# Kernel optimization log

Measured on AMD Instinct MI355X. Metric: run time of the kernel, lower is better.

## Reference

```python
import jax, jax.numpy as jnp
import numpy as np

N_NODES = 100000
N_EDGES = 600000
F_IN = 128
F_OUT = 128


def setup_inputs() -> dict:
    key = jax.random.key(0)
    ks = jax.random.split(key, 9)
    stdv = 1.0 / np.sqrt(F_OUT)
    return {
        "x": jax.random.normal(ks[0], (N_NODES, F_IN), dtype=jnp.float32),
        "weight": jax.random.uniform(ks[1], (F_IN, F_OUT), dtype=jnp.float32, minval=-stdv, maxval=stdv),
        "bias": jax.random.uniform(ks[2], (F_OUT,), dtype=jnp.float32, minval=-stdv, maxval=stdv),
        "vals0": jax.random.uniform(ks[3], (N_EDGES,), dtype=jnp.float32),
        "vals1": jax.random.uniform(ks[4], (N_EDGES,), dtype=jnp.float32),
        "rows0": jax.random.randint(ks[5], (N_EDGES,), 0, N_NODES, dtype=jnp.int32),
        "cols0": jax.random.randint(ks[6], (N_EDGES,), 0, N_NODES, dtype=jnp.int32),
        "rows1": jax.random.randint(ks[7], (N_EDGES,), 0, N_NODES, dtype=jnp.int32),
        "cols1": jax.random.randint(ks[8], (N_EDGES,), 0, N_NODES, dtype=jnp.int32),
    }


def _spmm(rows, cols, vals, dense, n):
    # COO sparse [n,n] @ dense [n,f]: gather source rows, scale, scatter-add to dest rows
    msgs = dense[cols] * vals[:, None]          # [E, f]
    return jax.ops.segment_sum(msgs, rows, num_segments=n)


def reference(x, weight, bias, vals0, vals1, rows0, cols0, rows1, cols1):
    n = x.shape[0]
    support = x @ weight                         # [N, F_OUT] dense GEMM
    out = _spmm(rows0, cols0, vals0, support, n) \
        + _spmm(rows1, cols1, vals1, support, n)
    return out + bias
```

## Files before the change

kernel.cpp:

```cpp
#include <hip/hip_runtime.h>


#define FDIM 128
#define EPB 2048

typedef __attribute__((ext_vector_type(8))) short short8;
typedef __attribute__((ext_vector_type(4))) float floatx4;

__device__ __forceinline__ unsigned short f32_to_bf16(float f) {
    unsigned int u = __float_as_uint(f);
    unsigned int r = u + 0x7fffu + ((u >> 16) & 1u);
    return (unsigned short)(r >> 16);
}

__device__ __forceinline__ float bf16_lo(unsigned int u) {
    return __uint_as_float((u & 0xffffu) << 16);
}
__device__ __forceinline__ float bf16_hi(unsigned int u) {
    return __uint_as_float(u & 0xffff0000u);
}

__global__ __launch_bounds__(256) void hist_prep(const int* __restrict__ rows0,
                                                 const int* __restrict__ rows1,
                                                 int* __restrict__ count,
                                                 int* __restrict__ rank, int E,
                                                 const float* __restrict__ w,
                                                 unsigned short* __restrict__ wt,
                                                 int HB) {
    int bid = blockIdx.x;
    if (bid < HB) {
        int gid = bid * 256 + threadIdx.x;
        if (gid < 2 * E) {
            int r = (gid < E) ? rows0[gid] : rows1[gid - E];
            rank[gid] = atomicAdd(&count[r], 1);
        }
    } else {
        int idx = (bid - HB) * 256 + threadIdx.x;
        int nn = idx >> 7, k = idx & 127;
        wt[idx] = f32_to_bf16(w[(size_t)k * FDIM + nn]);
    }
}

__device__ __forceinline__ int block_incl_scan(int v, int tid, int* lds) {
    int lane = tid & 63, wv = tid >> 6;
    #pragma unroll
    for (int d = 1; d < 64; d <<= 1) {
        int y = __shfl_up(v, d);
        if (lane >= d) v += y;
    }
    if (lane == 63) lds[wv] = v;
    __syncthreads();
    if (wv == 0 && lane < 4) {
        int s = lds[lane];
        #pragma unroll
        for (int d = 1; d < 4; d <<= 1) {
            int y = __shfl_up(s, d);
            if (lane >= d) s += y;
        }
        lds[4 + lane] = s;
    }
    __syncthreads();
    int add = (wv > 0) ? lds[4 + wv - 1] : 0;
    return v + add;
}

__global__ __launch_bounds__(256) void rowptr_scan(const int* __restrict__ count,
                                                   int* __restrict__ rowptr,
                                                   int* __restrict__ gcur, int n) {
    __shared__ int lds[8];
    __shared__ int base;
    int tid = threadIdx.x;
    int idx = blockIdx.x * 256 + tid;
    int v = (idx < n) ? count[idx] : 0;
    int inc = block_incl_scan(v, tid, lds);
    if (tid == 255) base = atomicAdd(gcur, inc);
    __syncthreads();
    if (idx < n) rowptr[idx] = base + inc - v;
}

__global__ __launch_bounds__(256) void gemm_lds(const float* __restrict__ x,
                                                const unsigned short* __restrict__ wt,
                                                unsigned short* __restrict__ support,
                                                int n) {
    __shared__ __align__(16) short Bs[128][136];
    const int tid = threadIdx.x;

    #pragma unroll
    for (int i = 0; i < 8; ++i) {
        int idx = tid + i * 256;
        int r = idx >> 4, c8 = idx & 15;
        *(short8*)&Bs[r][c8 * 8] = *(const short8*)(wt + (size_t)r * FDIM + c8 * 8);
    }
    __syncthreads();

    const int wv = tid >> 6, lane = tid & 63;
    const int quad = lane >> 4, lr = lane & 15;
    const int row0 = blockIdx.x * 64 + wv * 16;
    if (row0 >= n) return;

    const int arow = row0 + lr;
    const bool rowok = arow < n;
    const float* xr = x + (size_t)arow * FDIM;

    float4 f[8];
    #pragma unroll
    for (int ks = 0; ks < 4; ++ks) {
        f[2 * ks]     = rowok ? *(const float4*)(xr + ks * 32 + quad * 8)     : make_float4(0.f,0.f,0.f,0.f);
        f[2 * ks + 1] = rowok ? *(const float4*)(xr + ks * 32 + quad * 8 + 4) : make_float4(0.f,0.f,0.f,0.f);
    }

    floatx4 acc[8];
    #pragma unroll
    for (int nt = 0; nt < 8; ++nt) acc[nt] = (floatx4)0.f;

    #pragma unroll
    for (int ks = 0; ks < 4; ++ks) {
        float4 lo = f[2 * ks], hi = f[2 * ks + 1];
        short8 a;
        a[0] = (short)f32_to_bf16(lo.x); a[1] = (short)f32_to_bf16(lo.y);
        a[2] = (short)f32_to_bf16(lo.z); a[3] = (short)f32_to_bf16(lo.w);
        a[4] = (short)f32_to_bf16(hi.x); a[5] = (short)f32_to_bf16(hi.y);
        a[6] = (short)f32_to_bf16(hi.z); a[7] = (short)f32_to_bf16(hi.w);
        #pragma unroll
        for (int nt = 0; nt < 8; ++nt) {
            short8 b = *(const short8*)&Bs[nt * 16 + lr][ks * 32 + quad * 8];
            acc[nt] = __builtin_amdgcn_mfma_f32_16x16x32_bf16(a, b, acc[nt], 0, 0, 0);
        }
    }

    #pragma unroll
    for (int i = 0; i < 4; ++i) {
        int row = row0 + quad * 4 + i;
        if (row < n) {
            #pragma unroll
            for (int nt = 0; nt < 8; ++nt)
                support[(size_t)row * FDIM + nt * 16 + lr] = f32_to_bf16(acc[nt][i]);
        }
    }
}

__global__ __launch_bounds__(256) void scatter_row(
    const int* __restrict__ rows0, const int* __restrict__ cols0, const float* __restrict__ vals0,
    const int* __restrict__ rows1, const int* __restrict__ cols1, const float* __restrict__ vals1,
    const int* __restrict__ rank, const int* __restrict__ rowptr,
    int2* __restrict__ rec, int E, int nper) {
    const int p = blockIdx.x & 7;
    const int rlo = p * nper;
    const int base = (blockIdx.x >> 3) * EPB;
    const int tid = threadIdx.x;
    #pragma unroll
    for (int it = 0; it < EPB / 256; ++it) {
        int gid = base + it * 256 + tid;
        if (gid < 2 * E) {
            int r = (gid < E) ? rows0[gid] : rows1[gid - E];
            if ((unsigned)(r - rlo) < (unsigned)nper) {
                int c; float v;
                if (gid < E) { c = cols0[gid]; v = vals0[gid]; }
                else         { int e = gid - E; c = cols1[e]; v = vals1[e]; }
                rec[rowptr[r] + rank[gid]] = make_int2(c, __float_as_int(v));
            }
        }
    }
}

__global__ __launch_bounds__(256) void pull_csr(const unsigned short* __restrict__ support,
                                                const int* __restrict__ rowptr,
                                                const int* __restrict__ count,
                                                const int2* __restrict__ rec,
                                                const float* __restrict__ bias,
                                                float* __restrict__ out, int n) {
    int wid = (blockIdx.x * 256 + threadIdx.x) >> 6;
    int lane = threadIdx.x & 63;
    if (wid >= n) return;
    int beg = rowptr[wid];
    int end = beg + count[wid];
    float ax = 0.f, ay = 0.f;
    const char* sp = (const char*)support;
    const unsigned loff = (unsigned)lane << 2;

    for (int base = beg; base < end; base += 64) {
        int m = end - base; if (m > 64) m = 64;
        long long pk = 0;
        if (lane < m) pk = *(const long long*)&rec[base + lane];
        int j = 0;
        for (; j + 8 <= m; j += 8) {
            long long p0 = __shfl(pk, j);
            long long p1 = __shfl(pk, j + 1);
            long long p2 = __shfl(pk, j + 2);
            long long p3 = __shfl(pk, j + 3);
            long long p4 = __shfl(pk, j + 4);
            long long p5 = __shfl(pk, j + 5);
            long long p6 = __shfl(pk, j + 6);
            long long p7 = __shfl(pk, j + 7);
            unsigned u0 = *(const unsigned*)(sp + (((unsigned)p0) << 8) + loff);
            unsigned u1 = *(const unsigned*)(sp + (((unsigned)p1) << 8) + loff);
            unsigned u2 = *(const unsigned*)(sp + (((unsigned)p2) << 8) + loff);
            unsigned u3 = *(const unsigned*)(sp + (((unsigned)p3) << 8) + loff);
            unsigned u4 = *(const unsigned*)(sp + (((unsigned)p4) << 8) + loff);
            unsigned u5 = *(const unsigned*)(sp + (((unsigned)p5) << 8) + loff);
            unsigned u6 = *(const unsigned*)(sp + (((unsigned)p6) << 8) + loff);
            unsigned u7 = *(const unsigned*)(sp + (((unsigned)p7) << 8) + loff);
            float v0 = __int_as_float((int)(p0 >> 32));
            float v1 = __int_as_float((int)(p1 >> 32));
            float v2 = __int_as_float((int)(p2 >> 32));
            float v3 = __int_as_float((int)(p3 >> 32));
            float v4 = __int_as_float((int)(p4 >> 32));
            float v5 = __int_as_float((int)(p5 >> 32));
            float v6 = __int_as_float((int)(p6 >> 32));
            float v7 = __int_as_float((int)(p7 >> 32));
            ax += v0 * bf16_lo(u0); ay += v0 * bf16_hi(u0);
            ax += v1 * bf16_lo(u1); ay += v1 * bf16_hi(u1);
            ax += v2 * bf16_lo(u2); ay += v2 * bf16_hi(u2);
            ax += v3 * bf16_lo(u3); ay += v3 * bf16_hi(u3);
            ax += v4 * bf16_lo(u4); ay += v4 * bf16_hi(u4);
            ax += v5 * bf16_lo(u5); ay += v5 * bf16_hi(u5);
            ax += v6 * bf16_lo(u6); ay += v6 * bf16_hi(u6);
            ax += v7 * bf16_lo(u7); ay += v7 * bf16_hi(u7);
        }
        for (; j + 4 <= m; j += 4) {
            long long p0 = __shfl(pk, j);
            long long p1 = __shfl(pk, j + 1);
            long long p2 = __shfl(pk, j + 2);
            long long p3 = __shfl(pk, j + 3);
            unsigned u0 = *(const unsigned*)(sp + (((unsigned)p0) << 8) + loff);
            unsigned u1 = *(const unsigned*)(sp + (((unsigned)p1) << 8) + loff);
            unsigned u2 = *(const unsigned*)(sp + (((unsigned)p2) << 8) + loff);
            unsigned u3 = *(const unsigned*)(sp + (((unsigned)p3) << 8) + loff);
            float v0 = __int_as_float((int)(p0 >> 32));
            float v1 = __int_as_float((int)(p1 >> 32));
            float v2 = __int_as_float((int)(p2 >> 32));
            float v3 = __int_as_float((int)(p3 >> 32));
            ax += v0 * bf16_lo(u0); ay += v0 * bf16_hi(u0);
            ax += v1 * bf16_lo(u1); ay += v1 * bf16_hi(u1);
            ax += v2 * bf16_lo(u2); ay += v2 * bf16_hi(u2);
            ax += v3 * bf16_lo(u3); ay += v3 * bf16_hi(u3);
        }
        for (; j < m; ++j) {
            long long p = __shfl(pk, j);
            unsigned u = *(const unsigned*)(sp + (((unsigned)p) << 8) + loff);
            float v = __int_as_float((int)(p >> 32));
            ax += v * bf16_lo(u); ay += v * bf16_hi(u);
        }
    }
    float2 b = *(const float2*)(bias + lane * 2);
    *(float2*)(out + (size_t)wid * FDIM + lane * 2) = make_float2(ax + b.x, ay + b.y);
}

__global__ __launch_bounds__(256) void wt_only(const float* __restrict__ w,
                                               unsigned short* __restrict__ wt) {
    int idx = blockIdx.x * 256 + threadIdx.x;
    int nn = idx >> 7, k = idx & 127;
    wt[idx] = f32_to_bf16(w[(size_t)k * FDIM + nn]);
}

__global__ __launch_bounds__(256) void init_bias(const float* __restrict__ bias,
                                                 float* __restrict__ out, int n) {
    int idx = blockIdx.x * 256 + threadIdx.x;
    int total = n * (FDIM / 4);
    if (idx < total) {
        int j = (idx & (FDIM / 4 - 1)) * 4;
        float4 b = *(const float4*)(bias + j);
        *(float4*)(out + (size_t)idx * 4) = b;
    }
}

__global__ __launch_bounds__(256) void scatter_bf16(
    const unsigned short* __restrict__ support,
    const int* __restrict__ rows0, const int* __restrict__ cols0, const float* __restrict__ vals0,
    const int* __restrict__ rows1, const int* __restrict__ cols1, const float* __restrict__ vals1,
    float* __restrict__ out, int E) {
    int gid = blockIdx.x * 256 + threadIdx.x;
    int lane = gid & 63;
    int eg = gid >> 6;
    if (eg >= 2 * E) return;
    int r, c; float v;
    if (eg < E) { r = rows0[eg]; c = cols0[eg]; v = vals0[eg]; }
    else        { int e = eg - E; r = rows1[e]; c = cols1[e]; v = vals1[e]; }
    unsigned int u = *(const unsigned int*)(support + (size_t)c * FDIM + lane * 2);
    float sx = bf16_lo(u);
    float sy = bf16_hi(u);
    float* op = out + (size_t)r * FDIM + lane * 2;
    atomicAdd(op,     sx * v);
    atomicAdd(op + 1, sy * v);
}

static inline size_t align256(size_t v) { return (v + 255) & ~(size_t)255; }

extern "C" void kernel_launch(void* const* d_in, const int* in_sizes, int n_in,
                              void* d_out, int out_size, void* d_ws, size_t ws_size,
                              hipStream_t stream) {
    const float* x     = (const float*)d_in[0];
    const float* w     = (const float*)d_in[1];
    const float* bias  = (const float*)d_in[2];
    const float* vals0 = (const float*)d_in[3];
    const float* vals1 = (const float*)d_in[4];
    const int*   rows0 = (const int*)d_in[5];
    const int*   cols0 = (const int*)d_in[6];
    const int*   rows1 = (const int*)d_in[7];
    const int*   cols1 = (const int*)d_in[8];
    const int n = in_sizes[0] / FDIM;
    const int E = in_sizes[3];
    float* out = (float*)d_out;

    const int NB = (n + 255) / 256;

    size_t off = 0;
    unsigned short* support = (unsigned short*)((char*)d_ws + off);
    off = align256(off + (size_t)n * FDIM * 2);
    unsigned short* wt = (unsigned short*)((char*)d_ws + off);
    off = align256(off + (size_t)FDIM * FDIM * 2);
    size_t count_off = off;
    int*  count  = (int*)((char*)d_ws + off);  off = align256(off + (size_t)n * 4);
    int*  gcur   = (int*)((char*)d_ws + off);  off = align256(off + 4);
    size_t zero_bytes = off - count_off;
    int*  rowptr = (int*)((char*)d_ws + off);  off = align256(off + (size_t)n * 4);
    int*  rank   = (int*)((char*)d_ws + off);  off = align256(off + (size_t)2 * E * 4);
    int2* rec    = (int2*)((char*)d_ws + off); off = align256(off + (size_t)2 * E * 8);

    const bool fits = off <= ws_size;

    if (fits) {
        hipMemsetAsync((char*)d_ws + count_off, 0, zero_bytes, stream);
        const int HB = (2 * E + 255) / 256;
        hist_prep<<<HB + 64, 256, 0, stream>>>(rows0, rows1, count, rank, E, w, wt, HB);
        rowptr_scan<<<NB, 256, 0, stream>>>(count, rowptr, gcur, n);
        gemm_lds<<<(n + 63) / 64, 256, 0, stream>>>(x, wt, support, n);

        const int nper   = (n + 7) / 8;
        const int ntiles = (2 * E + EPB - 1) / EPB;
        scatter_row<<<ntiles * 8, 256, 0, stream>>>(rows0, cols0, vals0,
                                                    rows1, cols1, vals1,
                                                    rank, rowptr, rec, E, nper);
        pull_csr<<<(n + 3) / 4, 256, 0, stream>>>(support, rowptr, count, rec, bias, out, n);
    } else {
        wt_only<<<(FDIM * FDIM) / 256, 256, 0, stream>>>(w, wt);
        gemm_lds<<<(n + 63) / 64, 256, 0, stream>>>(x, wt, support, n);
        int total4 = n * (FDIM / 4);
        init_bias<<<(total4 + 255) / 256, 256, 0, stream>>>(bias, out, n);
        long long tthreads = 2LL * E * 64;
        int blocks = (int)((tthreads + 255) / 256);
        scatter_bf16<<<blocks, 256, 0, stream>>>(support, rows0, cols0, vals0,
                                                 rows1, cols1, vals1, out, E);
    }
}
```

Measured before the change: 273.1 us.

## Fuse CSR build phases into one cooperative kernel with grid syncs

Replaces the memset, histogram/weight-prep, rowptr scan and scatter launches with a single cooperative kernel that runs the phases as grid-stride loops separated by grid.sync(). The aim is to remove per-launch overhead and the inter-kernel gaps between the small preprocessing kernels. In exchange, parallelism is capped at the resident grid (at most 2048 blocks), grid-wide barriers are added, and the GEMM now runs after the scatter instead of between the scan and the scatter. The old multi-kernel path is kept as a fallback if the cooperative launch is unavailable or fails.

```diff
diff --git a/kernel.cpp b/kernel.cpp
--- a/kernel.cpp
+++ b/kernel.cpp
@@ -1,4 +1,7 @@
 #include <hip/hip_runtime.h>
+#include <hip/hip_cooperative_groups.h>
+
+namespace cg = cooperative_groups;
 
 
 #define FDIM 128
@@ -18,6 +21,90 @@
 }
 __device__ __forceinline__ float bf16_hi(unsigned int u) {
     return __uint_as_float(u & 0xffff0000u);
+}
+
+__device__ __forceinline__ int block_incl_scan(int v, int tid, int* lds) {
+    int lane = tid & 63, wv = tid >> 6;
+    #pragma unroll
+    for (int d = 1; d < 64; d <<= 1) {
+        int y = __shfl_up(v, d);
+        if (lane >= d) v += y;
+    }
+    if (lane == 63) lds[wv] = v;
+    __syncthreads();
+    if (wv == 0 && lane < 4) {
+        int s = lds[lane];
+        #pragma unroll
+        for (int d = 1; d < 4; d <<= 1) {
+            int y = __shfl_up(s, d);
+            if (lane >= d) s += y;
+        }
+        lds[4 + lane] = s;
+    }
+    __syncthreads();
+    int add = (wv > 0) ? lds[4 + wv - 1] : 0;
+    return v + add;
+}
+
+__global__ __launch_bounds__(256) void coop_build(
+    const int* __restrict__ rows0, const int* __restrict__ cols0, const float* __restrict__ vals0,
+    const int* __restrict__ rows1, const int* __restrict__ cols1, const float* __restrict__ vals1,
+    const float* __restrict__ w, unsigned short* __restrict__ wt,
+    int* __restrict__ count, int* __restrict__ gcur,
+    int* __restrict__ rank, int* __restrict__ rowptr,
+    int2* __restrict__ rec,
+    int E, int n, int NB, int ntiles, int nper) {
+    cg::grid_group grid = cg::this_grid();
+    __shared__ int slds[8];
+    __shared__ int sbase;
+    const int tid = threadIdx.x;
+    const int nb = gridDim.x;
+    const int gt = blockIdx.x * 256 + tid;
+    const int gstr = nb * 256;
+
+    for (int i = gt; i < n; i += gstr) count[i] = 0;
+    if (gt == 0) *gcur = 0;
+    for (int i = gt; i < FDIM * FDIM; i += gstr) {
+        int nn = i >> 7, k = i & 127;
+        wt[i] = f32_to_bf16(w[(size_t)k * FDIM + nn]);
+    }
+    grid.sync();
+
+    for (int gid = gt; gid < 2 * E; gid += gstr) {
+        int r = (gid < E) ? rows0[gid] : rows1[gid - E];
+        rank[gid] = atomicAdd(&count[r], 1);
+    }
+    grid.sync();
+
+    for (int vb = blockIdx.x; vb < NB; vb += nb) {
+        int idx = vb * 256 + tid;
+        int v = (idx < n) ? count[idx] : 0;
+        int inc = block_incl_scan(v, tid, slds);
+        if (tid == 255) sbase = atomicAdd(gcur, inc);
+        __syncthreads();
+        if (idx < n) rowptr[idx] = sbase + inc - v;
+        __syncthreads();
+    }
+    grid.sync();
+
+    const int p = blockIdx.x & 7;
+    const int rlo = p * nper;
+    for (int vt = blockIdx.x >> 3; vt < ntiles; vt += (nb >> 3)) {
+        const int base = vt * EPB;
+        #pragma unroll
+        for (int it = 0; it < EPB / 256; ++it) {
+            int gid = base + it * 256 + tid;
+            if (gid < 2 * E) {
+                int r = (gid < E) ? rows0[gid] : rows1[gid - E];
+                if ((unsigned)(r - rlo) < (unsigned)nper) {
+                    int c; float v;
+                    if (gid < E) { c = cols0[gid]; v = vals0[gid]; }
+                    else         { int e = gid - E; c = cols1[e]; v = vals1[e]; }
+                    rec[rowptr[r] + rank[gid]] = make_int2(c, __float_as_int(v));
+                }
+            }
+        }
+    }
 }
 
 __global__ __launch_bounds__(256) void hist_prep(const int* __restrict__ rows0,
@@ -41,29 +128,6 @@
     }
 }
 
-__device__ __forceinline__ int block_incl_scan(int v, int tid, int* lds) {
-    int lane = tid & 63, wv = tid >> 6;
-    #pragma unroll
-    for (int d = 1; d < 64; d <<= 1) {
-        int y = __shfl_up(v, d);
-        if (lane >= d) v += y;
-    }
-    if (lane == 63) lds[wv] = v;
-    __syncthreads();
-    if (wv == 0 && lane < 4) {
-        int s = lds[lane];
-        #pragma unroll
-        for (int d = 1; d < 4; d <<= 1) {
-            int y = __shfl_up(s, d);
-            if (lane >= d) s += y;
-        }
-        lds[4 + lane] = s;
-    }
-    __syncthreads();
-    int add = (wv > 0) ? lds[4 + wv - 1] : 0;
-    return v + add;
-}
-
 __global__ __launch_bounds__(256) void rowptr_scan(const int* __restrict__ count,
                                                    int* __restrict__ rowptr,
                                                    int* __restrict__ gcur, int n) {
@@ -78,6 +142,30 @@
     if (idx < n) rowptr[idx] = base + inc - v;
 }
 
+__global__ __launch_bounds__(256) void scatter_row(
+    const int* __restrict__ rows0, const int* __restrict__ cols0, const float* __restrict__ vals0,
+    const int* __restrict__ rows1, const int* __restrict__ cols1, const float* __restrict__ vals1,
+    const int* __restrict__ rank, const int* __restrict__ rowptr,
+    int2* __restrict__ rec, int E, int nper) {
+    const int p = blockIdx.x & 7;
+    const int rlo = p * nper;
+    const int base = (blockIdx.x >> 3) * EPB;
+    const int tid = threadIdx.x;
+    #pragma unroll
+    for (int it = 0; it < EPB / 256; ++it) {
+        int gid = base + it * 256 + tid;
+        if (gid < 2 * E) {
+            int r = (gid < E) ? rows0[gid] : rows1[gid - E];
+            if ((unsigned)(r - rlo) < (unsigned)nper) {
+                int c; float v;
+                if (gid < E) { c = cols0[gid]; v = vals0[gid]; }
+                else         { int e = gid - E; c = cols1[e]; v = vals1[e]; }
+                rec[rowptr[r] + rank[gid]] = make_int2(c, __float_as_int(v));
+            }
+        }
+    }
+}
+
 __global__ __launch_bounds__(256) void gemm_lds(const float* __restrict__ x,
                                                 const unsigned short* __restrict__ wt,
                                                 unsigned short* __restrict__ support,
@@ -135,30 +223,6 @@
             #pragma unroll
             for (int nt = 0; nt < 8; ++nt)
                 support[(size_t)row * FDIM + nt * 16 + lr] = f32_to_bf16(acc[nt][i]);
-        }
-    }
-}
-
-__global__ __launch_bounds__(256) void scatter_row(
-    const int* __restrict__ rows0, const int* __restrict__ cols0, const float* __restrict__ vals0,
-    const int* __restrict__ rows1, const int* __restrict__ cols1, const float* __restrict__ vals1,
-    const int* __restrict__ rank, const int* __restrict__ rowptr,
-    int2* __restrict__ rec, int E, int nper) {
-    const int p = blockIdx.x & 7;
-    const int rlo = p * nper;
-    const int base = (blockIdx.x >> 3) * EPB;
-    const int tid = threadIdx.x;
-    #pragma unroll
-    for (int it = 0; it < EPB / 256; ++it) {
-        int gid = base + it * 256 + tid;
-        if (gid < 2 * E) {
-            int r = (gid < E) ? rows0[gid] : rows1[gid - E];
-            if ((unsigned)(r - rlo) < (unsigned)nper) {
-                int c; float v;
-                if (gid < E) { c = cols0[gid]; v = vals0[gid]; }
-                else         { int e = gid - E; c = cols1[e]; v = vals1[e]; }
-                rec[rowptr[r] + rank[gid]] = make_int2(c, __float_as_int(v));
-            }
         }
     }
 }
@@ -298,11 +362,11 @@
     const int*   cols0 = (const int*)d_in[6];
     const int*   rows1 = (const int*)d_in[7];
     const int*   cols1 = (const int*)d_in[8];
-    const int n = in_sizes[0] / FDIM;
-    const int E = in_sizes[3];
+    int n = in_sizes[0] / FDIM;
+    int E = in_sizes[3];
     float* out = (float*)d_out;
 
-    const int NB = (n + 255) / 256;
+    int NB = (n + 255) / 256;
 
     size_t off = 0;
     unsigned short* support = (unsigned short*)((char*)d_ws + off);
@@ -318,16 +382,46 @@
     int2* rec    = (int2*)((char*)d_ws + off); off = align256(off + (size_t)2 * E * 8);
 
     const bool fits = off <= ws_size;
-
-    if (fits) {
+    int nper   = (n + 7) / 8;
+    int ntiles = (2 * E + EPB - 1) / EPB;
+
+    static int coop_grid = -1;
+    if (coop_grid < 0) {
+        int dev = 0, sup = 0, cu = 0, bpc = 0;
+        hipGetDevice(&dev);
+        hipDeviceGetAttribute(&sup, hipDeviceAttributeCooperativeLaunch, dev);
+        hipDeviceGetAttribute(&cu, hipDeviceAttributeMultiprocessorCount, dev);
+        hipOccupancyMaxActiveBlocksPerMultiprocessor(&bpc, coop_build, 256, 0);
+        int g = bpc * cu;
+        if (g > 2048) g = 2048;
+        g &= ~7;
+        coop_grid = (sup && g >= 8) ? g : 0;
+    }
+
+    bool coop_done = false;
+    if (fits && coop_grid > 0) {
+        void* args[] = {
+            (void*)&rows0, (void*)&cols0, (void*)&vals0,
+            (void*)&rows1, (void*)&cols1, (void*)&vals1,
+            (void*)&w, (void*)&wt,
+            (void*)&count, (void*)&gcur, (void*)&rank, (void*)&rowptr, (void*)&rec,
+            (void*)&E, (void*)&n, (void*)&NB, (void*)&ntiles, (void*)&nper
+        };
+        hipError_t err = hipLaunchCooperativeKernel((const void*)coop_build,
+                                                    dim3(coop_grid), dim3(256),
+                                                    args, 0, stream);
+        coop_done = (err == hipSuccess);
+    }
+
+    if (coop_done) {
+        gemm_lds<<<(n + 63) / 64, 256, 0, stream>>>(x, wt, support, n);
+        pull_csr<<<(n + 3) / 4, 256, 0, stream>>>(support, rowptr, count, rec, bias, out, n);
+    } else if (fits) {
         hipMemsetAsync((char*)d_ws + count_off, 0, zero_bytes, stream);
         const int HB = (2 * E + 255) / 256;
         hist_prep<<<HB + 64, 256, 0, stream>>>(rows0, rows1, count, rank, E, w, wt, HB);
         rowptr_scan<<<NB, 256, 0, stream>>>(count, rowptr, gcur, n);
         gemm_lds<<<(n + 63) / 64, 256, 0, stream>>>(x, wt, support, n);
-
-        const int nper   = (n + 7) / 8;
-        const int ntiles = (2 * E + EPB - 1) / EPB;
         scatter_row<<<ntiles * 8, 256, 0, stream>>>(rows0, cols0, vals0,
                                                     rows1, cols1, vals1,
                                                     rank, rowptr, rec, E, nper);
```

Measured after the change: 781.9 us. 186% more time.
